# Kernel optimization log

Hardware: AMD Instinct MI355X
Metric: run time of the kernel (lower is better)

## Reference

```python
import jax, jax.numpy as jnp
import numpy as np

B, L, D, H, DK, DV = 2, 2048, 512, 8, 64, 64
EPS_LN = 1e-6


def setup_inputs() -> dict:
    key = jax.random.key(0)
    ks = jax.random.split(key, 14)
    ws = 0.02  # weight init scale
    inp = {}
    for i, n in enumerate(["q_r", "q_i", "k_r", "k_i", "v_r", "v_i"]):
        inp[n] = jax.random.normal(ks[i], (B, L, D), jnp.float32)
    for j, n in enumerate(["wq_r", "wq_i", "wk_r", "wk_i", "wv_r", "wv_i", "fc_r", "fc_i"]):
        inp[n] = jax.random.normal(ks[6 + j], (D, D), jnp.float32) * ws
    # complextorch CVLayerNorm affine: (2,2,D) weight, diag = 1/sqrt(2); complex bias = 0
    c = np.float32(1.0 / np.sqrt(2.0))
    ln_w = jnp.zeros((2, 2, D), jnp.float32).at[0, 0].set(c).at[1, 1].set(c)
    inp["ln_w"] = ln_w
    inp["ln_b_r"] = jnp.zeros((D,), jnp.float32)
    inp["ln_b_i"] = jnp.zeros((D,), jnp.float32)
    return inp


def _cv_layernorm(x, ln_w, ln_b_r, ln_b_i):
    # covariance-whitening complex LayerNorm over last dim (complextorch style)
    xr, xi = jnp.real(x), jnp.imag(x)
    xr = xr - jnp.mean(xr, axis=-1, keepdims=True)
    xi = xi - jnp.mean(xi, axis=-1, keepdims=True)
    vrr = jnp.mean(xr * xr, axis=-1, keepdims=True) + EPS_LN
    vii = jnp.mean(xi * xi, axis=-1, keepdims=True) + EPS_LN
    vri = jnp.mean(xr * xi, axis=-1, keepdims=True)
    s = jnp.sqrt(vrr * vii - vri * vri)
    t = jnp.sqrt(vrr + vii + 2.0 * s)
    inv = 1.0 / (s * t)
    rrr, rii, rri = (vii + s) * inv, (vrr + s) * inv, -vri * inv
    yr = rrr * xr + rri * xi
    yi = rri * xr + rii * xi
    out_r = ln_w[0, 0] * yr + ln_w[0, 1] * yi + ln_b_r
    out_i = ln_w[1, 0] * yr + ln_w[1, 1] * yi + ln_b_i
    return out_r, out_i


def _mha(q_r, q_i, k_r, k_i, v_r, v_i, wq_r, wq_i, wk_r, wk_i, wv_r, wv_i,
         fc_r, fc_i, ln_w, ln_b_r, ln_b_i):
    q = (q_r + 1j * q_i).astype(jnp.complex64)
    k = (k_r + 1j * k_i).astype(jnp.complex64)
    v = (v_r + 1j * v_i).astype(jnp.complex64)
    Wq = (wq_r + 1j * wq_i).astype(jnp.complex64)
    Wk = (wk_r + 1j * wk_i).astype(jnp.complex64)
    Wv = (wv_r + 1j * wv_i).astype(jnp.complex64)
    Wfc = (fc_r + 1j * fc_i).astype(jnp.complex64)
    b, lq = q.shape[0], q.shape[1]
    # complex linear projections (torch Linear: y = x @ W^T), split into heads
    qh = jnp.einsum('bld,ed->ble', q, Wq).reshape(b, lq, H, DK).transpose(0, 2, 1, 3)
    kh = jnp.einsum('bld,ed->ble', k, Wk).reshape(b, -1, H, DK).transpose(0, 2, 1, 3)
    vh = jnp.einsum('bld,ed->ble', v, Wv).reshape(b, -1, H, DV).transpose(0, 2, 1, 3)
    temp = jnp.float32(DK ** 0.5)
    attn = jnp.einsum('bhqd,bhkd->bhqk', qh / temp, kh)  # [B,H,Lq,Lk] complex
    # CVSoftMax: softmax over magnitude, phase preserved
    mag = jnp.abs(attn)
    w = jax.nn.softmax(mag, axis=-1)
    attn = (w * jnp.exp(1j * jnp.angle(attn))).astype(jnp.complex64)
    out = jnp.einsum('bhqk,bhkd->bhqd', attn, vh)
    out = out.transpose(0, 2, 1, 3).reshape(b, lq, H * DV)
    out = jnp.einsum('ble,de->bld', out, Wfc)
    x = out + q  # residual (dropout is identity at p=0 / eval)
    return _cv_layernorm(x, ln_w, ln_b_r, ln_b_i)


def reference(q_r, q_i, k_r, k_i, v_r, v_i, wq_r, wq_i, wk_r, wk_i, wv_r, wv_i,
              fc_r, fc_i, ln_w, ln_b_r, ln_b_i):
    out_r, out_i = _mha(q_r, q_i, k_r, k_i, v_r, v_i, wq_r, wq_i, wk_r, wk_i,
                        wv_r, wv_i, fc_r, fc_i, ln_w, ln_b_r, ln_b_i)
    # stack real/imag so output is a real float32 tensor [B, L, D, 2]
    return jnp.stack([out_r, out_i], axis=-1)
```

## Files before the change

### kernel.cpp

```cpp
#include <hip/hip_runtime.h>
#include <hip/hip_bf16.h>
#include <math.h>

#define NB 2
#define NL 2048
#define ND 512
#define NH 8
#define NDK 64
#define NROW (NB*NL)
#define HEADSZ (NB*NH*NL*NDK)
#define SEG_BIG ((size_t)NROW*ND)

typedef __attribute__((ext_vector_type(8))) short bf16x8;
typedef __attribute__((ext_vector_type(4))) float f32x4;

__device__ __align__(16) short g_bq_r[HEADSZ], g_bq_i[HEADSZ];
__device__ __align__(16) short g_bk_r[HEADSZ], g_bk_i[HEADSZ];
__device__ __align__(16) short g_bv_r[HEADSZ], g_bv_i[HEADSZ];
__device__ __align__(16) short g_bo_r[SEG_BIG], g_bo_i[SEG_BIG];
__device__ float g_x_r[SEG_BIG];
__device__ float g_x_i[SEG_BIG];
__device__ __align__(16) unsigned g_po[(size_t)2*16*NL*NDK];
__device__ float g_pw[(size_t)2*16*NL];

static __device__ __forceinline__ unsigned pack_bf2(float lo, float hi) {
    __hip_bfloat162 h = __float22bfloat162_rn(make_float2(lo, hi));
    unsigned u;
    __builtin_memcpy(&u, &h, 4);
    return u;
}
static __device__ __forceinline__ float bf_lo(unsigned u) {
    const unsigned v = u << 16;
    float f; __builtin_memcpy(&f, &v, 4);
    return f;
}
static __device__ __forceinline__ float bf_hi(unsigned u) {
    const unsigned v = u & 0xFFFF0000u;
    float f; __builtin_memcpy(&f, &v, 4);
    return f;
}
static __device__ __forceinline__ uint4 ld_cvt(const float* p) {
    const float4 a = *(const float4*)p;
    const float4 b = *(const float4*)(p + 4);
    uint4 o;
    o.x = pack_bf2(a.x, a.y); o.y = pack_bf2(a.z, a.w);
    o.z = pack_bf2(b.x, b.y); o.w = pack_bf2(b.z, b.w);
    return o;
}
static __device__ __forceinline__ bf16x8 negbf(bf16x8 v) {
    #pragma unroll
    for (int e = 0; e < 8; ++e) v[e] ^= (short)0x8000;
    return v;
}

struct GPtrs {
    const float* xr[3]; const float* xi[3];
    const float* wr[4]; const float* wi[4];
    const float* rr; const float* ri;
};

template<int MODE>
__global__ __launch_bounds__(256, 2)
void bgemm(GPtrs gp)
{
    __shared__ __align__(16) short sAr[64][64], sAi[64][64];
    __shared__ __align__(16) short sBr[64][64], sBi[64][64];

    const int bm = blockIdx.x, bn = blockIdx.y;
    const int which = (MODE == 0) ? blockIdx.z : 3;
    const int tx = threadIdx.x;
    const int wave = tx >> 6, lane = tx & 63;
    const int l15 = lane & 15, l4 = lane >> 4;

    const float* Xr = nullptr;
    const float* Xi = nullptr;
    if constexpr (MODE == 0) { Xr = gp.xr[which]; Xi = gp.xi[which]; }
    const float* Wr = gp.wr[which];
    const float* Wi = gp.wi[which];

    const int t0r = tx >> 3;
    const int t0g = tx & 7;

    f32x4 Cr[4] = {}, Ci[4] = {};

    for (int kk = 0; kk < ND; kk += 64) {
        uint4 va0, va1, va2, va3, vb0, vb1, vb2, vb3;
        {
            const size_t a0 = (size_t)(bm*64 + t0r)*ND + kk + t0g*8;
            const size_t a1 = a0 + (size_t)32*ND;
            if constexpr (MODE == 0) {
                va0 = ld_cvt(Xr + a0); va1 = ld_cvt(Xi + a0);
                va2 = ld_cvt(Xr + a1); va3 = ld_cvt(Xi + a1);
            } else {
                va0 = *(const uint4*)(g_bo_r + a0); va1 = *(const uint4*)(g_bo_i + a0);
                va2 = *(const uint4*)(g_bo_r + a1); va3 = *(const uint4*)(g_bo_i + a1);
            }
            const size_t b0 = (size_t)(bn*64 + t0r)*ND + kk + t0g*8;
            const size_t b1 = b0 + (size_t)32*ND;
            vb0 = ld_cvt(Wr + b0); vb1 = ld_cvt(Wi + b0);
            vb2 = ld_cvt(Wr + b1); vb3 = ld_cvt(Wi + b1);
        }
        __syncthreads();
        {
            const int g0 = (t0g ^ (t0r & 7)) << 3;
            const int g1 = (t0g ^ ((t0r + 32) & 7)) << 3;
            *(uint4*)&sAr[t0r][g0]    = va0;
            *(uint4*)&sAi[t0r][g0]    = va1;
            *(uint4*)&sAr[t0r+32][g1] = va2;
            *(uint4*)&sAi[t0r+32][g1] = va3;
            *(uint4*)&sBr[t0r][g0]    = vb0;
            *(uint4*)&sBi[t0r][g0]    = vb1;
            *(uint4*)&sBr[t0r+32][g1] = vb2;
            *(uint4*)&sBi[t0r+32][g1] = vb3;
        }
        __syncthreads();

        #pragma unroll
        for (int ks = 0; ks < 2; ++ks) {
            const int arow = 16*wave + l15;
            const int ag = ((ks*4 + l4) ^ (arow & 7)) << 3;
            const bf16x8 aAr = *(const bf16x8*)&sAr[arow][ag];
            const bf16x8 aAi = *(const bf16x8*)&sAi[arow][ag];
            const bf16x8 aAn = negbf(aAi);
            #pragma unroll
            for (int nt = 0; nt < 4; ++nt) {
                const int brow = nt*16 + l15;
                const int bg = ((ks*4 + l4) ^ (brow & 7)) << 3;
                const bf16x8 bBr = *(const bf16x8*)&sBr[brow][bg];
                const bf16x8 bBi = *(const bf16x8*)&sBi[brow][bg];
                Cr[nt] = __builtin_amdgcn_mfma_f32_16x16x32_bf16(aAr, bBr, Cr[nt], 0, 0, 0);
                Cr[nt] = __builtin_amdgcn_mfma_f32_16x16x32_bf16(aAn, bBi, Cr[nt], 0, 0, 0);
                Ci[nt] = __builtin_amdgcn_mfma_f32_16x16x32_bf16(aAr, bBi, Ci[nt], 0, 0, 0);
                Ci[nt] = __builtin_amdgcn_mfma_f32_16x16x32_bf16(aAi, bBr, Ci[nt], 0, 0, 0);
            }
        }
    }

    const int m0 = bm*64 + 16*wave + 4*l4;
    if constexpr (MODE == 0) {
        if (which == 2) {
            const int bb = m0 >> 11, ll = m0 & (NL-1);
            const int c = ll >> 5, lgrp = (ll >> 3) & 3, e = ll & 7;
            #pragma unroll
            for (int nt = 0; nt < 4; ++nt) {
                const int d = nt*16 + l15;
                const int r = d & 31, dpart = d >> 5;
                const int p = (4*dpart + lgrp) ^ (r & 7);
                const size_t off = (size_t)(bb*NH + bn)*(NL*NDK) + (size_t)c*2048 + (r*8 + p)*8 + e;
                *(uint2*)(g_bv_r + off) = make_uint2(pack_bf2(Cr[nt][0], Cr[nt][1]),
                                                     pack_bf2(Cr[nt][2], Cr[nt][3]));
                *(uint2*)(g_bv_i + off) = make_uint2(pack_bf2(Ci[nt][0], Ci[nt][1]),
                                                     pack_bf2(Ci[nt][2], Ci[nt][3]));
            }
        } else {
            const float s = (which == 0) ? 0.125f : 1.0f;
            short* Pr = (which == 0) ? g_bq_r : g_bk_r;
            short* Pi = (which == 0) ? g_bq_i : g_bk_i;
            #pragma unroll
            for (int r = 0; r < 4; ++r) {
                const int m = m0 + r;
                const int bb = m >> 11, ll = m & (NL-1);
                const size_t base = ((size_t)(bb*NH + bn)*NL + ll)*NDK;
                #pragma unroll
                for (int nt = 0; nt < 4; ++nt) {
                    int col = nt*16 + l15;
                    if (which == 1)
                        col = (col & 7) | ((((col >> 3) ^ (ll & 7))) << 3);
                    const unsigned pk = pack_bf2(Cr[nt][r]*s, Ci[nt][r]*s);
                    Pr[base + col] = (short)(pk & 0xFFFFu);
                    Pi[base + col] = (short)(pk >> 16);
                }
            }
        }
    } else {
        const float* Rr = gp.rr;
        const float* Ri = gp.ri;
        #pragma unroll
        for (int r = 0; r < 4; ++r) {
            const int m = m0 + r;
            const size_t base = (size_t)m*ND + bn*64;
            #pragma unroll
            for (int nt = 0; nt < 4; ++nt) {
                const size_t idx = base + nt*16 + l15;
                g_x_r[idx] = Cr[nt][r] + Rr[idx];
                g_x_i[idx] = Ci[nt][r] + Ri[idx];
            }
        }
    }
}

__global__ __launch_bounds__(256, 4)
void cattn()
{
    __shared__ __align__(16) short sKV[2][8192];
    __shared__ __align__(16) short sCr[64][32], sCi[64][32];

    const int nb = blockIdx.x;
    const int xcd = nb & 7, rest = nb >> 3;
    const int bh = xcd*2 + (rest >> 6);
    const int within = rest & 63;
    const int q0 = (within >> 1) * 64;
    const int half = within & 1;

    const int tx = threadIdx.x;
    const int wave = tx >> 6, lane = tx & 63;
    const int l15 = lane & 15, l4 = lane >> 4;

    const short* Kr = g_bk_r + (size_t)bh*NL*NDK;
    const short* Ki = g_bk_i + (size_t)bh*NL*NDK;
    const short* Vr = g_bv_r + (size_t)bh*NL*NDK;
    const short* Vi = g_bv_i + (size_t)bh*NL*NDK;

    bf16x8 aQr[2], aQi[2], aQn[2];
    {
        const size_t qb = ((size_t)bh*NL + q0 + 16*wave + l15)*NDK + 8*l4;
        aQr[0] = *(const bf16x8*)(g_bq_r + qb);
        aQr[1] = *(const bf16x8*)(g_bq_r + qb + 32);
        aQi[0] = *(const bf16x8*)(g_bq_i + qb);
        aQi[1] = *(const bf16x8*)(g_bq_i + qb + 32);
        aQn[0] = negbf(aQi[0]); aQn[1] = negbf(aQi[1]);
    }

    f32x4 Or[4] = {}, Oi[4] = {};
    float ws[4] = {0.f, 0.f, 0.f, 0.f};

    const short* kvplane = (wave == 0) ? Kr : (wave == 1) ? Ki : (wave == 2) ? Vr : Vi;
    const int pbase = wave * 2048;

    #define STAGE_KV(CHUNK, BUF) do {                                         \
        _Pragma("unroll")                                                     \
        for (int i_ = 0; i_ < 4; ++i_) {                                      \
            const int u_ = i_*64 + lane;                                      \
            __builtin_amdgcn_global_load_lds(                                 \
                (const __attribute__((address_space(1))) void*)               \
                    (kvplane + (size_t)(CHUNK)*2048 + (size_t)u_*8),          \
                (__attribute__((address_space(3))) void*)                     \
                    &sKV[BUF][pbase + u_*8], 16, 0, 0);                       \
        }                                                                     \
    } while (0)

    const int cbase = half * 32;
    STAGE_KV(cbase, 0);
    asm volatile("s_waitcnt vmcnt(0)" ::: "memory");
    __syncthreads();

    const float LOG2E = 1.44269504f;
    const float SHIFT = -4.0f*1.44269504f;

    for (int t = 0; t < 32; ++t) {
        const int cur = t & 1, nxt = cur ^ 1;
        if (t < 31) STAGE_KV(cbase + t + 1, nxt);

        #pragma unroll
        for (int tt = 0; tt < 2; ++tt) {
            const int row = tt*16 + l15;
            const int swb = row & 7;
            f32x4 Sr = {}, Si = {};
            __builtin_amdgcn_s_setprio(1);
            #pragma unroll
            for (int c = 0; c < 2; ++c) {
                const int off = (((c*4 + l4) ^ swb) << 3);
                const bf16x8 bKr = *(const bf16x8*)&sKV[cur][row*64 + off];
                const bf16x8 bKi = *(const bf16x8*)&sKV[cur][2048 + row*64 + off];
                Sr = __builtin_amdgcn_mfma_f32_16x16x32_bf16(aQr[c], bKr, Sr, 0, 0, 0);
                Sr = __builtin_amdgcn_mfma_f32_16x16x32_bf16(aQn[c], bKi, Sr, 0, 0, 0);
                Si = __builtin_amdgcn_mfma_f32_16x16x32_bf16(aQr[c], bKi, Si, 0, 0, 0);
                Si = __builtin_amdgcn_mfma_f32_16x16x32_bf16(aQi[c], bKr, Si, 0, 0, 0);
            }
            __builtin_amdgcn_s_setprio(0);
            const int kgrp = row >> 3;
            #pragma unroll
            for (int r = 0; r < 4; ++r) {
                const int qrow = 16*wave + 4*l4 + r;
                const float s2 = fmaxf(fmaf(Sr[r], Sr[r], Si[r]*Si[r]), 1e-30f);
                const float irs = __builtin_amdgcn_rsqf(s2);
                const float mag = s2 * irs;
                const float w = exp2f(fmaf(mag, LOG2E, SHIFT));
                const float sc = w * irs;
                ws[r] += w;
                const int col = (row & 7) | ((kgrp ^ ((qrow >> 2) & 3)) << 3);
                const unsigned pk = pack_bf2(Sr[r]*sc, Si[r]*sc);
                sCr[qrow][col] = (short)(pk & 0xFFFFu);
                sCi[qrow][col] = (short)(pk >> 16);
            }
        }

        asm volatile("s_waitcnt lgkmcnt(0)" ::: "memory");
        __builtin_amdgcn_sched_barrier(0);

        bf16x8 aCr, aCi, aCn;
        {
            const int qrow = 16*wave + l15;
            const int off = (l4 ^ ((qrow >> 2) & 3)) << 3;
            aCr = *(const bf16x8*)&sCr[qrow][off];
            aCi = *(const bf16x8*)&sCi[qrow][off];
            aCn = negbf(aCi);
        }
        __builtin_amdgcn_s_setprio(1);
        #pragma unroll
        for (int tt = 0; tt < 4; ++tt) {
            const int d = tt*16 + l15;
            const int r = d & 31, dpart = tt >> 1;
            const int p = (4*dpart + l4) ^ (r & 7);
            const int vb = r*64 + p*8;
            const bf16x8 bVr = *(const bf16x8*)&sKV[cur][4096 + vb];
            const bf16x8 bVi = *(const bf16x8*)&sKV[cur][6144 + vb];
            Or[tt] = __builtin_amdgcn_mfma_f32_16x16x32_bf16(aCr, bVr, Or[tt], 0, 0, 0);
            Or[tt] = __builtin_amdgcn_mfma_f32_16x16x32_bf16(aCn, bVi, Or[tt], 0, 0, 0);
            Oi[tt] = __builtin_amdgcn_mfma_f32_16x16x32_bf16(aCr, bVi, Oi[tt], 0, 0, 0);
            Oi[tt] = __builtin_amdgcn_mfma_f32_16x16x32_bf16(aCi, bVr, Oi[tt], 0, 0, 0);
        }
        __builtin_amdgcn_s_setprio(0);

        asm volatile("s_waitcnt vmcnt(0)" ::: "memory");
        __syncthreads();
    }

    #pragma unroll
    for (int r = 0; r < 4; ++r) {
        #pragma unroll
        for (int off = 8; off; off >>= 1) ws[r] += __shfl_xor(ws[r], off);
    }
    const size_t pb = (size_t)(half*16 + bh)*NL;
    if (l15 == 0) {
        #pragma unroll
        for (int r = 0; r < 4; ++r)
            g_pw[pb + q0 + 16*wave + 4*l4 + r] = ws[r];
    }
    #pragma unroll
    for (int tt = 0; tt < 4; ++tt) {
        const int d = tt*16 + l15;
        #pragma unroll
        for (int r = 0; r < 4; ++r) {
            const int q = q0 + 16*wave + 4*l4 + r;
            g_po[(pb + q)*NDK + d] = pack_bf2(Or[tt][r], Oi[tt][r]);
        }
    }
    #undef STAGE_KV
}

__global__ __launch_bounds__(256)
void comb()
{
    const size_t t4 = ((size_t)blockIdx.x*256 + threadIdx.x) * 4;
    const int d = (int)(t4 & 63);
    const int q = (int)((t4 >> 6) & (NL-1));
    const int bh = (int)(t4 >> 17);
    const size_t p = ((size_t)bh*NL + q)*NDK + d;
    const uint4 a = *(const uint4*)&g_po[p];
    const uint4 c = *(const uint4*)&g_po[(size_t)16*NL*NDK + p];
    const float w = g_pw[(size_t)bh*NL + q] + g_pw[(size_t)(16 + bh)*NL + q];
    const float inv = 1.0f / w;
    float fr[4], fi[4];
    fr[0] = (bf_lo(a.x) + bf_lo(c.x))*inv; fi[0] = (bf_hi(a.x) + bf_hi(c.x))*inv;
    fr[1] = (bf_lo(a.y) + bf_lo(c.y))*inv; fi[1] = (bf_hi(a.y) + bf_hi(c.y))*inv;
    fr[2] = (bf_lo(a.z) + bf_lo(c.z))*inv; fi[2] = (bf_hi(a.z) + bf_hi(c.z))*inv;
    fr[3] = (bf_lo(a.w) + bf_lo(c.w))*inv; fi[3] = (bf_hi(a.w) + bf_hi(c.w))*inv;
    const int b = bh >> 3, h = bh & 7;
    const size_t o = ((size_t)b*NL + q)*ND + h*NDK + d;
    *(uint2*)(g_bo_r + o) = make_uint2(pack_bf2(fr[0], fr[1]), pack_bf2(fr[2], fr[3]));
    *(uint2*)(g_bo_i + o) = make_uint2(pack_bf2(fi[0], fi[1]), pack_bf2(fi[2], fi[3]));
}

__global__ __launch_bounds__(256)
void cvln(const float* __restrict__ ln_w, const float* __restrict__ lnb_r,
          const float* __restrict__ lnb_i, float2* __restrict__ out)
{
    __shared__ float red[4][5];
    const int row = blockIdx.x, tx = threadIdx.x;
    const float* xr = g_x_r + (size_t)row*ND;
    const float* xi = g_x_i + (size_t)row*ND;
    const float a0 = xr[tx], a1 = xr[tx+256];
    const float b0 = xi[tx], b1 = xi[tx+256];
    float s_r = a0 + a1, s_i = b0 + b1;
    float srr = a0*a0 + a1*a1, sii = b0*b0 + b1*b1, sri = a0*b0 + a1*b1;
    #pragma unroll
    for (int off = 32; off; off >>= 1) {
        s_r += __shfl_xor(s_r, off);  s_i += __shfl_xor(s_i, off);
        srr += __shfl_xor(srr, off);  sii += __shfl_xor(sii, off);
        sri += __shfl_xor(sri, off);
    }
    const int wave = tx >> 6, lane = tx & 63;
    if (lane == 0) { red[wave][0]=s_r; red[wave][1]=s_i; red[wave][2]=srr; red[wave][3]=sii; red[wave][4]=sri; }
    __syncthreads();
    s_r = red[0][0]+red[1][0]+red[2][0]+red[3][0];
    s_i = red[0][1]+red[1][1]+red[2][1]+red[3][1];
    srr = red[0][2]+red[1][2]+red[2][2]+red[3][2];
    sii = red[0][3]+red[1][3]+red[2][3]+red[3][3];
    sri = red[0][4]+red[1][4]+red[2][4]+red[3][4];

    const float invD = 1.0f/ND;
    const float mr = s_r*invD, mi = s_i*invD;
    const float vrr = srr*invD - mr*mr + 1e-6f;
    const float vii = sii*invD - mi*mi + 1e-6f;
    const float vri = sri*invD - mr*mi;
    const float s  = sqrtf(vrr*vii - vri*vri);
    const float t  = sqrtf(vrr + vii + 2.0f*s);
    const float inv = 1.0f/(s*t);
    const float rrr = (vii + s)*inv, rii = (vrr + s)*inv, rri = -vri*inv;

    #pragma unroll
    for (int p = 0; p < 2; ++p) {
        const int d = tx + p*256;
        const float cxr = (p ? a1 : a0) - mr;
        const float cxi = (p ? b1 : b0) - mi;
        const float yr = rrr*cxr + rri*cxi;
        const float yi = rri*cxr + rii*cxi;
        const float w00 = ln_w[d], w01 = ln_w[512 + d];
        const float w10 = ln_w[1024 + d], w11 = ln_w[1536 + d];
        out[(size_t)row*ND + d] = make_float2(w00*yr + w01*yi + lnb_r[d],
                                              w10*yr + w11*yi + lnb_i[d]);
    }
}

extern "C" void kernel_launch(void* const* d_in, const int* in_sizes, int n_in,
                              void* d_out, int out_size, void* d_ws, size_t ws_size,
                              hipStream_t stream)
{
    (void)in_sizes; (void)n_in; (void)d_ws; (void)ws_size; (void)out_size;
    const float* ln_w = (const float*)d_in[14];
    const float* lnbr = (const float*)d_in[15];
    const float* lnbi = (const float*)d_in[16];

    GPtrs gp;
    gp.xr[0] = (const float*)d_in[0];  gp.xi[0] = (const float*)d_in[1];
    gp.xr[1] = (const float*)d_in[2];  gp.xi[1] = (const float*)d_in[3];
    gp.xr[2] = (const float*)d_in[4];  gp.xi[2] = (const float*)d_in[5];
    gp.wr[0] = (const float*)d_in[6];  gp.wi[0] = (const float*)d_in[7];
    gp.wr[1] = (const float*)d_in[8];  gp.wi[1] = (const float*)d_in[9];
    gp.wr[2] = (const float*)d_in[10]; gp.wi[2] = (const float*)d_in[11];
    gp.wr[3] = (const float*)d_in[12]; gp.wi[3] = (const float*)d_in[13];
    gp.rr = (const float*)d_in[0];     gp.ri = (const float*)d_in[1];

    bgemm<0><<<dim3(NROW/64, ND/64, 3), 256, 0, stream>>>(gp);
    cattn<<<1024, 256, 0, stream>>>();
    comb<<<2048, 256, 0, stream>>>();
    bgemm<1><<<dim3(NROW/64, ND/64), 256, 0, stream>>>(gp);
    cvln<<<NROW, 256, 0, stream>>>(ln_w, lnbr, lnbi, (float2*)d_out);
}
```

Measured before the change: 171.1 us.

## Enlarge complex GEMM M-tile to 128 rows with two MFMA row tiles per wave

The projection and output GEMMs now compute a 128x64 tile per block instead of 64x64. Each wave handles two 16-row A sub-tiles and reuses the B fragments it loads from shared memory across both. This cuts weight reloads from global memory and shared-memory B reads per MFMA, and halves the grid. The cost is more registers (accumulators doubled), more LDS, and fewer blocks (768 for the projection, 256 for the output GEMM), which may reduce occupancy and load balance.

```diff
diff --git a/kernel.cpp b/kernel.cpp
--- a/kernel.cpp
+++ b/kernel.cpp
@@ -63,8 +63,8 @@
 __global__ __launch_bounds__(256, 2)
 void bgemm(GPtrs gp)
 {
-    __shared__ __align__(16) short sAr[64][64], sAi[64][64];
-    __shared__ __align__(16) short sBr[64][64], sBi[64][64];
+    __shared__ __align__(16) short sAr[128][64], sAi[128][64];
+    __shared__ __align__(16) short sBr[64][64],  sBi[64][64];
 
     const int bm = blockIdx.x, bn = blockIdx.y;
     const int which = (MODE == 0) ? blockIdx.z : 3;
@@ -81,109 +81,123 @@
     const int t0r = tx >> 3;
     const int t0g = tx & 7;
 
-    f32x4 Cr[4] = {}, Ci[4] = {};
+    f32x4 Cr[2][4] = {}, Ci[2][4] = {};
 
     for (int kk = 0; kk < ND; kk += 64) {
-        uint4 va0, va1, va2, va3, vb0, vb1, vb2, vb3;
-        {
-            const size_t a0 = (size_t)(bm*64 + t0r)*ND + kk + t0g*8;
-            const size_t a1 = a0 + (size_t)32*ND;
+        uint4 va[8], vb[4];
+        #pragma unroll
+        for (int p = 0; p < 4; ++p) {
+            const size_t a = (size_t)(bm*128 + t0r + p*32)*ND + kk + t0g*8;
             if constexpr (MODE == 0) {
-                va0 = ld_cvt(Xr + a0); va1 = ld_cvt(Xi + a0);
-                va2 = ld_cvt(Xr + a1); va3 = ld_cvt(Xi + a1);
+                va[p]   = ld_cvt(Xr + a);
+                va[4+p] = ld_cvt(Xi + a);
             } else {
-                va0 = *(const uint4*)(g_bo_r + a0); va1 = *(const uint4*)(g_bo_i + a0);
-                va2 = *(const uint4*)(g_bo_r + a1); va3 = *(const uint4*)(g_bo_i + a1);
-            }
-            const size_t b0 = (size_t)(bn*64 + t0r)*ND + kk + t0g*8;
-            const size_t b1 = b0 + (size_t)32*ND;
-            vb0 = ld_cvt(Wr + b0); vb1 = ld_cvt(Wi + b0);
-            vb2 = ld_cvt(Wr + b1); vb3 = ld_cvt(Wi + b1);
+                va[p]   = *(const uint4*)(g_bo_r + a);
+                va[4+p] = *(const uint4*)(g_bo_i + a);
+            }
+        }
+        #pragma unroll
+        for (int p = 0; p < 2; ++p) {
+            const size_t bo = (size_t)(bn*64 + t0r + p*32)*ND + kk + t0g*8;
+            vb[p]   = ld_cvt(Wr + bo);
+            vb[2+p] = ld_cvt(Wi + bo);
         }
         __syncthreads();
-        {
-            const int g0 = (t0g ^ (t0r & 7)) << 3;
-            const int g1 = (t0g ^ ((t0r + 32) & 7)) << 3;
-            *(uint4*)&sAr[t0r][g0]    = va0;
-            *(uint4*)&sAi[t0r][g0]    = va1;
-            *(uint4*)&sAr[t0r+32][g1] = va2;
-            *(uint4*)&sAi[t0r+32][g1] = va3;
-            *(uint4*)&sBr[t0r][g0]    = vb0;
-            *(uint4*)&sBi[t0r][g0]    = vb1;
-            *(uint4*)&sBr[t0r+32][g1] = vb2;
-            *(uint4*)&sBi[t0r+32][g1] = vb3;
+        #pragma unroll
+        for (int p = 0; p < 4; ++p) {
+            const int row = t0r + p*32;
+            const int g = (t0g ^ (row & 7)) << 3;
+            *(uint4*)&sAr[row][g] = va[p];
+            *(uint4*)&sAi[row][g] = va[4+p];
+        }
+        #pragma unroll
+        for (int p = 0; p < 2; ++p) {
+            const int row = t0r + p*32;
+            const int g = (t0g ^ (row & 7)) << 3;
+            *(uint4*)&sBr[row][g] = vb[p];
+            *(uint4*)&sBi[row][g] = vb[2+p];
         }
         __syncthreads();
 
         #pragma unroll
         for (int ks = 0; ks < 2; ++ks) {
-            const int arow = 16*wave + l15;
-            const int ag = ((ks*4 + l4) ^ (arow & 7)) << 3;
-            const bf16x8 aAr = *(const bf16x8*)&sAr[arow][ag];
-            const bf16x8 aAi = *(const bf16x8*)&sAi[arow][ag];
-            const bf16x8 aAn = negbf(aAi);
+            bf16x8 bB_r[4], bB_i[4];
             #pragma unroll
             for (int nt = 0; nt < 4; ++nt) {
                 const int brow = nt*16 + l15;
                 const int bg = ((ks*4 + l4) ^ (brow & 7)) << 3;
-                const bf16x8 bBr = *(const bf16x8*)&sBr[brow][bg];
-                const bf16x8 bBi = *(const bf16x8*)&sBi[brow][bg];
-                Cr[nt] = __builtin_amdgcn_mfma_f32_16x16x32_bf16(aAr, bBr, Cr[nt], 0, 0, 0);
-                Cr[nt] = __builtin_amdgcn_mfma_f32_16x16x32_bf16(aAn, bBi, Cr[nt], 0, 0, 0);
-                Ci[nt] = __builtin_amdgcn_mfma_f32_16x16x32_bf16(aAr, bBi, Ci[nt], 0, 0, 0);
-                Ci[nt] = __builtin_amdgcn_mfma_f32_16x16x32_bf16(aAi, bBr, Ci[nt], 0, 0, 0);
-            }
-        }
-    }
-
-    const int m0 = bm*64 + 16*wave + 4*l4;
-    if constexpr (MODE == 0) {
-        if (which == 2) {
-            const int bb = m0 >> 11, ll = m0 & (NL-1);
-            const int c = ll >> 5, lgrp = (ll >> 3) & 3, e = ll & 7;
+                bB_r[nt] = *(const bf16x8*)&sBr[brow][bg];
+                bB_i[nt] = *(const bf16x8*)&sBi[brow][bg];
+            }
             #pragma unroll
-            for (int nt = 0; nt < 4; ++nt) {
-                const int d = nt*16 + l15;
-                const int r = d & 31, dpart = d >> 5;
-                const int p = (4*dpart + lgrp) ^ (r & 7);
-                const size_t off = (size_t)(bb*NH + bn)*(NL*NDK) + (size_t)c*2048 + (r*8 + p)*8 + e;
-                *(uint2*)(g_bv_r + off) = make_uint2(pack_bf2(Cr[nt][0], Cr[nt][1]),
-                                                     pack_bf2(Cr[nt][2], Cr[nt][3]));
-                *(uint2*)(g_bv_i + off) = make_uint2(pack_bf2(Ci[nt][0], Ci[nt][1]),
-                                                     pack_bf2(Ci[nt][2], Ci[nt][3]));
+            for (int mi = 0; mi < 2; ++mi) {
+                const int arow = 32*wave + 16*mi + l15;
+                const int ag = ((ks*4 + l4) ^ (arow & 7)) << 3;
+                const bf16x8 aAr = *(const bf16x8*)&sAr[arow][ag];
+                const bf16x8 aAi = *(const bf16x8*)&sAi[arow][ag];
+                const bf16x8 aAn = negbf(aAi);
+                #pragma unroll
+                for (int nt = 0; nt < 4; ++nt) {
+                    Cr[mi][nt] = __builtin_amdgcn_mfma_f32_16x16x32_bf16(aAr, bB_r[nt], Cr[mi][nt], 0, 0, 0);
+                    Cr[mi][nt] = __builtin_amdgcn_mfma_f32_16x16x32_bf16(aAn, bB_i[nt], Cr[mi][nt], 0, 0, 0);
+                    Ci[mi][nt] = __builtin_amdgcn_mfma_f32_16x16x32_bf16(aAr, bB_i[nt], Ci[mi][nt], 0, 0, 0);
+                    Ci[mi][nt] = __builtin_amdgcn_mfma_f32_16x16x32_bf16(aAi, bB_r[nt], Ci[mi][nt], 0, 0, 0);
+                }
+            }
+        }
+    }
+
+    #pragma unroll
+    for (int mi = 0; mi < 2; ++mi) {
+        const int m0 = bm*128 + 32*wave + 16*mi + 4*l4;
+        if constexpr (MODE == 0) {
+            if (which == 2) {
+                const int bb = m0 >> 11, ll = m0 & (NL-1);
+                const int c = ll >> 5, lgrp = (ll >> 3) & 3, e = ll & 7;
+                #pragma unroll
+                for (int nt = 0; nt < 4; ++nt) {
+                    const int d = nt*16 + l15;
+                    const int r = d & 31, dpart = d >> 5;
+                    const int p = (4*dpart + lgrp) ^ (r & 7);
+                    const size_t off = (size_t)(bb*NH + bn)*(NL*NDK) + (size_t)c*2048 + (r*8 + p)*8 + e;
+                    *(uint2*)(g_bv_r + off) = make_uint2(pack_bf2(Cr[mi][nt][0], Cr[mi][nt][1]),
+                                                         pack_bf2(Cr[mi][nt][2], Cr[mi][nt][3]));
+                    *(uint2*)(g_bv_i + off) = make_uint2(pack_bf2(Ci[mi][nt][0], Ci[mi][nt][1]),
+                                                         pack_bf2(Ci[mi][nt][2], Ci[mi][nt][3]));
+                }
+            } else {
+                const float s = (which == 0) ? 0.125f : 1.0f;
+                short* Pr = (which == 0) ? g_bq_r : g_bk_r;
+                short* Pi = (which == 0) ? g_bq_i : g_bk_i;
+                #pragma unroll
+                for (int r = 0; r < 4; ++r) {
+                    const int m = m0 + r;
+                    const int bb = m >> 11, ll = m & (NL-1);
+                    const size_t base = ((size_t)(bb*NH + bn)*NL + ll)*NDK;
+                    #pragma unroll
+                    for (int nt = 0; nt < 4; ++nt) {
+                        int col = nt*16 + l15;
+                        if (which == 1)
+                            col = (col & 7) | ((((col >> 3) ^ (ll & 7))) << 3);
+                        const unsigned pk = pack_bf2(Cr[mi][nt][r]*s, Ci[mi][nt][r]*s);
+                        Pr[base + col] = (short)(pk & 0xFFFFu);
+                        Pi[base + col] = (short)(pk >> 16);
+                    }
+                }
             }
         } else {
-            const float s = (which == 0) ? 0.125f : 1.0f;
-            short* Pr = (which == 0) ? g_bq_r : g_bk_r;
-            short* Pi = (which == 0) ? g_bq_i : g_bk_i;
+            const float* Rr = gp.rr;
+            const float* Ri = gp.ri;
             #pragma unroll
             for (int r = 0; r < 4; ++r) {
                 const int m = m0 + r;
-                const int bb = m >> 11, ll = m & (NL-1);
-                const size_t base = ((size_t)(bb*NH + bn)*NL + ll)*NDK;
+                const size_t base = (size_t)m*ND + bn*64;
                 #pragma unroll
                 for (int nt = 0; nt < 4; ++nt) {
-                    int col = nt*16 + l15;
-                    if (which == 1)
-                        col = (col & 7) | ((((col >> 3) ^ (ll & 7))) << 3);
-                    const unsigned pk = pack_bf2(Cr[nt][r]*s, Ci[nt][r]*s);
-                    Pr[base + col] = (short)(pk & 0xFFFFu);
-                    Pi[base + col] = (short)(pk >> 16);
+                    const size_t idx = base + nt*16 + l15;
+                    g_x_r[idx] = Cr[mi][nt][r] + Rr[idx];
+                    g_x_i[idx] = Ci[mi][nt][r] + Ri[idx];
                 }
-            }
-        }
-    } else {
-        const float* Rr = gp.rr;
-        const float* Ri = gp.ri;
-        #pragma unroll
-        for (int r = 0; r < 4; ++r) {
-            const int m = m0 + r;
-            const size_t base = (size_t)m*ND + bn*64;
-            #pragma unroll
-            for (int nt = 0; nt < 4; ++nt) {
-                const size_t idx = base + nt*16 + l15;
-                g_x_r[idx] = Cr[nt][r] + Rr[idx];
-                g_x_i[idx] = Ci[nt][r] + Ri[idx];
             }
         }
     }
@@ -432,9 +446,9 @@
     gp.wr[3] = (const float*)d_in[12]; gp.wi[3] = (const float*)d_in[13];
     gp.rr = (const float*)d_in[0];     gp.ri = (const float*)d_in[1];
 
-    bgemm<0><<<dim3(NROW/64, ND/64, 3), 256, 0, stream>>>(gp);
+    bgemm<0><<<dim3(NROW/128, ND/64, 3), 256, 0, stream>>>(gp);
     cattn<<<1024, 256, 0, stream>>>();
     comb<<<2048, 256, 0, stream>>>();
-    bgemm<1><<<dim3(NROW/64, ND/64), 256, 0, stream>>>(gp);
+    bgemm<1><<<dim3(NROW/128, ND/64), 256, 0, stream>>>(gp);
     cvln<<<NROW, 256, 0, stream>>>(ln_w, lnbr, lnbi, (float2*)d_out);
 }
```

New measurement: 212.5 us. 1.24x slower.

## Pre-convert inputs to pre-swizzled bf16 and stream GEMM tiles via global_load_lds

Applied to the files above, without the earlier changes.

Adds a conversion kernel that turns all fp32 activations and weights into bf16 once, storing them with the XOR swizzle already applied, and makes the combine kernel write its output in the same layout. The GEMM kernels then fill shared memory with direct global-to-LDS loads, one plane per wave, instead of per-thread fp32 loads, in-register conversion and LDS stores. This removes the repeated fp32 reads and conversions inside the projection GEMM. In exchange it adds an extra launch and a full read/write pass over the inputs, plus a trailing barrier per k-step.

```diff
diff --git a/kernel.cpp b/kernel.cpp
--- a/kernel.cpp
+++ b/kernel.cpp
@@ -10,10 +10,13 @@
 #define NROW (NB*NL)
 #define HEADSZ (NB*NH*NL*NDK)
 #define SEG_BIG ((size_t)NROW*ND)
+#define SEG_SMALL ((size_t)ND*ND)
+#define TOT_CVT (6*SEG_BIG + 8*SEG_SMALL)
 
 typedef __attribute__((ext_vector_type(8))) short bf16x8;
 typedef __attribute__((ext_vector_type(4))) float f32x4;
 
+__device__ __align__(16) short g_bf[TOT_CVT];
 __device__ __align__(16) short g_bq_r[HEADSZ], g_bq_i[HEADSZ];
 __device__ __align__(16) short g_bk_r[HEADSZ], g_bk_i[HEADSZ];
 __device__ __align__(16) short g_bv_r[HEADSZ], g_bv_i[HEADSZ];
@@ -53,18 +56,29 @@
     return v;
 }
 
-struct GPtrs {
-    const float* xr[3]; const float* xi[3];
-    const float* wr[4]; const float* wi[4];
-    const float* rr; const float* ri;
-};
+struct SrcPtrs { const float* p[14]; };
+
+__global__ __launch_bounds__(256)
+void tobf(SrcPtrs sp)
+{
+    const size_t i = ((size_t)blockIdx.x*256 + threadIdx.x) * 8;
+    if (i >= TOT_CVT) return;
+    int seg; size_t off, sbase;
+    if (i < 6*SEG_BIG) { seg = (int)(i / SEG_BIG); off = i % SEG_BIG; sbase = (size_t)seg*SEG_BIG; }
+    else { const size_t j = i - 6*SEG_BIG; seg = 6 + (int)(j / SEG_SMALL); off = j % SEG_SMALL;
+           sbase = 6*SEG_BIG + (size_t)(seg-6)*SEG_SMALL; }
+    const uint4 v = ld_cvt(sp.p[seg] + off);
+    const int r7 = (int)(off >> 9) & 7;
+    const int g  = (int)(off >> 3) & 7;
+    const size_t dst = (off & ~(size_t)0x38) | ((size_t)(g ^ r7) << 3);
+    *(uint4*)(g_bf + sbase + dst) = v;
+}
 
 template<int MODE>
 __global__ __launch_bounds__(256, 2)
-void bgemm(GPtrs gp)
-{
-    __shared__ __align__(16) short sAr[64][64], sAi[64][64];
-    __shared__ __align__(16) short sBr[64][64], sBi[64][64];
+void bgemm(const float* __restrict__ Rr, const float* __restrict__ Ri)
+{
+    __shared__ __align__(16) short sAB[16384];
 
     const int bm = blockIdx.x, bn = blockIdx.y;
     const int which = (MODE == 0) ? blockIdx.z : 3;
@@ -72,68 +86,50 @@
     const int wave = tx >> 6, lane = tx & 63;
     const int l15 = lane & 15, l4 = lane >> 4;
 
-    const float* Xr = nullptr;
-    const float* Xi = nullptr;
-    if constexpr (MODE == 0) { Xr = gp.xr[which]; Xi = gp.xi[which]; }
-    const float* Wr = gp.wr[which];
-    const float* Wi = gp.wi[which];
-
-    const int t0r = tx >> 3;
-    const int t0g = tx & 7;
+    const short* Xr = (MODE == 0) ? g_bf + (size_t)(2*which)*SEG_BIG   : g_bo_r;
+    const short* Xi = (MODE == 0) ? g_bf + (size_t)(2*which+1)*SEG_BIG : g_bo_i;
+    const short* Wr = g_bf + 6*SEG_BIG + (size_t)(2*which)*SEG_SMALL;
+    const short* Wi = g_bf + 6*SEG_BIG + (size_t)(2*which+1)*SEG_SMALL;
+
+    const short* plane = (wave == 0) ? Xr : (wave == 1) ? Xi : (wave == 2) ? Wr : Wi;
+    const int prow0 = ((wave < 2) ? bm : bn) * 64;
+    const int pbase = wave * 4096;
 
     f32x4 Cr[4] = {}, Ci[4] = {};
 
     for (int kk = 0; kk < ND; kk += 64) {
-        uint4 va0, va1, va2, va3, vb0, vb1, vb2, vb3;
-        {
-            const size_t a0 = (size_t)(bm*64 + t0r)*ND + kk + t0g*8;
-            const size_t a1 = a0 + (size_t)32*ND;
-            if constexpr (MODE == 0) {
-                va0 = ld_cvt(Xr + a0); va1 = ld_cvt(Xi + a0);
-                va2 = ld_cvt(Xr + a1); va3 = ld_cvt(Xi + a1);
-            } else {
-                va0 = *(const uint4*)(g_bo_r + a0); va1 = *(const uint4*)(g_bo_i + a0);
-                va2 = *(const uint4*)(g_bo_r + a1); va3 = *(const uint4*)(g_bo_i + a1);
-            }
-            const size_t b0 = (size_t)(bn*64 + t0r)*ND + kk + t0g*8;
-            const size_t b1 = b0 + (size_t)32*ND;
-            vb0 = ld_cvt(Wr + b0); vb1 = ld_cvt(Wi + b0);
-            vb2 = ld_cvt(Wr + b1); vb3 = ld_cvt(Wi + b1);
-        }
-        __syncthreads();
-        {
-            const int g0 = (t0g ^ (t0r & 7)) << 3;
-            const int g1 = (t0g ^ ((t0r + 32) & 7)) << 3;
-            *(uint4*)&sAr[t0r][g0]    = va0;
-            *(uint4*)&sAi[t0r][g0]    = va1;
-            *(uint4*)&sAr[t0r+32][g1] = va2;
-            *(uint4*)&sAi[t0r+32][g1] = va3;
-            *(uint4*)&sBr[t0r][g0]    = vb0;
-            *(uint4*)&sBi[t0r][g0]    = vb1;
-            *(uint4*)&sBr[t0r+32][g1] = vb2;
-            *(uint4*)&sBi[t0r+32][g1] = vb3;
-        }
+        #pragma unroll
+        for (int i_ = 0; i_ < 8; ++i_) {
+            const int u_ = i_*64 + lane;
+            __builtin_amdgcn_global_load_lds(
+                (const __attribute__((address_space(1))) void*)
+                    (plane + (size_t)(prow0 + (u_ >> 3))*ND + kk + (u_ & 7)*8),
+                (__attribute__((address_space(3))) void*)
+                    &sAB[pbase + u_*8], 16, 0, 0);
+        }
+        asm volatile("s_waitcnt vmcnt(0)" ::: "memory");
         __syncthreads();
 
         #pragma unroll
         for (int ks = 0; ks < 2; ++ks) {
             const int arow = 16*wave + l15;
             const int ag = ((ks*4 + l4) ^ (arow & 7)) << 3;
-            const bf16x8 aAr = *(const bf16x8*)&sAr[arow][ag];
-            const bf16x8 aAi = *(const bf16x8*)&sAi[arow][ag];
+            const bf16x8 aAr = *(const bf16x8*)&sAB[arow*64 + ag];
+            const bf16x8 aAi = *(const bf16x8*)&sAB[4096 + arow*64 + ag];
             const bf16x8 aAn = negbf(aAi);
             #pragma unroll
             for (int nt = 0; nt < 4; ++nt) {
                 const int brow = nt*16 + l15;
                 const int bg = ((ks*4 + l4) ^ (brow & 7)) << 3;
-                const bf16x8 bBr = *(const bf16x8*)&sBr[brow][bg];
-                const bf16x8 bBi = *(const bf16x8*)&sBi[brow][bg];
+                const bf16x8 bBr = *(const bf16x8*)&sAB[8192  + brow*64 + bg];
+                const bf16x8 bBi = *(const bf16x8*)&sAB[12288 + brow*64 + bg];
                 Cr[nt] = __builtin_amdgcn_mfma_f32_16x16x32_bf16(aAr, bBr, Cr[nt], 0, 0, 0);
                 Cr[nt] = __builtin_amdgcn_mfma_f32_16x16x32_bf16(aAn, bBi, Cr[nt], 0, 0, 0);
                 Ci[nt] = __builtin_amdgcn_mfma_f32_16x16x32_bf16(aAr, bBi, Ci[nt], 0, 0, 0);
                 Ci[nt] = __builtin_amdgcn_mfma_f32_16x16x32_bf16(aAi, bBr, Ci[nt], 0, 0, 0);
             }
         }
+        __syncthreads();
     }
 
     const int m0 = bm*64 + 16*wave + 4*l4;
@@ -173,8 +169,6 @@
             }
         }
     } else {
-        const float* Rr = gp.rr;
-        const float* Ri = gp.ri;
         #pragma unroll
         for (int r = 0; r < 4; ++r) {
             const int m = m0 + r;
@@ -357,7 +351,8 @@
     fr[2] = (bf_lo(a.z) + bf_lo(c.z))*inv; fi[2] = (bf_hi(a.z) + bf_hi(c.z))*inv;
     fr[3] = (bf_lo(a.w) + bf_lo(c.w))*inv; fi[3] = (bf_hi(a.w) + bf_hi(c.w))*inv;
     const int b = bh >> 3, h = bh & 7;
-    const size_t o = ((size_t)b*NL + q)*ND + h*NDK + d;
+    const int dsw = ((((d >> 3) ^ (q & 7))) << 3) | (d & 7);
+    const size_t o = ((size_t)b*NL + q)*ND + h*NDK + dsw;
     *(uint2*)(g_bo_r + o) = make_uint2(pack_bf2(fr[0], fr[1]), pack_bf2(fr[2], fr[3]));
     *(uint2*)(g_bo_i + o) = make_uint2(pack_bf2(fi[0], fi[1]), pack_bf2(fi[2], fi[3]));
 }
@@ -418,23 +413,20 @@
                               hipStream_t stream)
 {
     (void)in_sizes; (void)n_in; (void)d_ws; (void)ws_size; (void)out_size;
+    const float* q_r  = (const float*)d_in[0];
+    const float* q_i  = (const float*)d_in[1];
     const float* ln_w = (const float*)d_in[14];
     const float* lnbr = (const float*)d_in[15];
     const float* lnbi = (const float*)d_in[16];
 
-    GPtrs gp;
-    gp.xr[0] = (const float*)d_in[0];  gp.xi[0] = (const float*)d_in[1];
-    gp.xr[1] = (const float*)d_in[2];  gp.xi[1] = (const float*)d_in[3];
-    gp.xr[2] = (const float*)d_in[4];  gp.xi[2] = (const float*)d_in[5];
-    gp.wr[0] = (const float*)d_in[6];  gp.wi[0] = (const float*)d_in[7];
-    gp.wr[1] = (const float*)d_in[8];  gp.wi[1] = (const float*)d_in[9];
-    gp.wr[2] = (const float*)d_in[10]; gp.wi[2] = (const float*)d_in[11];
-    gp.wr[3] = (const float*)d_in[12]; gp.wi[3] = (const float*)d_in[13];
-    gp.rr = (const float*)d_in[0];     gp.ri = (const float*)d_in[1];
-
-    bgemm<0><<<dim3(NROW/64, ND/64, 3), 256, 0, stream>>>(gp);
+    SrcPtrs sp;
+    for (int j = 0; j < 14; ++j) sp.p[j] = (const float*)d_in[j];
+
+    const int cvt_blocks = (int)((TOT_CVT/8 + 255)/256);
+    tobf<<<cvt_blocks, 256, 0, stream>>>(sp);
+    bgemm<0><<<dim3(NROW/64, ND/64, 3), 256, 0, stream>>>(nullptr, nullptr);
     cattn<<<1024, 256, 0, stream>>>();
     comb<<<2048, 256, 0, stream>>>();
-    bgemm<1><<<dim3(NROW/64, ND/64), 256, 0, stream>>>(gp);
+    bgemm<1><<<dim3(NROW/64, ND/64), 256, 0, stream>>>(q_r, q_i);
     cvln<<<NROW, 256, 0, stream>>>(ln_w, lnbr, lnbi, (float2*)d_out);
 }
```

Result: no change. 168.3 us (-1.6%).

## Pre-swizzle weights to bf16 and load GEMM tiles via direct global-to-LDS

Applied to the files above, without the earlier changes.

A new kernel converts all eight weight matrices to bf16 once per call and stores them in the pre-swizzled LDS layout. The GEMMs then fetch those tiles straight into shared memory with global_load_lds instead of loading fp32, converting and storing through registers. The attention-combine kernel now writes its output pre-swizzled so the output projection can use the same direct path. The residual sum is stored as packed bf16 real/imag pairs instead of two fp32 arrays, which cuts traffic into the layer norm at some precision cost, and the extra launch plus added barriers add overhead.

```diff
diff --git a/kernel.cpp b/kernel.cpp
--- a/kernel.cpp
+++ b/kernel.cpp
@@ -10,16 +10,18 @@
 #define NROW (NB*NL)
 #define HEADSZ (NB*NH*NL*NDK)
 #define SEG_BIG ((size_t)NROW*ND)
+#define SEG_SMALL ((size_t)ND*ND)
+#define TOT_W (8*SEG_SMALL)
 
 typedef __attribute__((ext_vector_type(8))) short bf16x8;
 typedef __attribute__((ext_vector_type(4))) float f32x4;
 
+__device__ __align__(16) short g_bfw[TOT_W];
 __device__ __align__(16) short g_bq_r[HEADSZ], g_bq_i[HEADSZ];
 __device__ __align__(16) short g_bk_r[HEADSZ], g_bk_i[HEADSZ];
 __device__ __align__(16) short g_bv_r[HEADSZ], g_bv_i[HEADSZ];
 __device__ __align__(16) short g_bo_r[SEG_BIG], g_bo_i[SEG_BIG];
-__device__ float g_x_r[SEG_BIG];
-__device__ float g_x_i[SEG_BIG];
+__device__ __align__(16) unsigned g_x[SEG_BIG];
 __device__ __align__(16) unsigned g_po[(size_t)2*16*NL*NDK];
 __device__ float g_pw[(size_t)2*16*NL];
 
@@ -55,16 +57,29 @@
 
 struct GPtrs {
     const float* xr[3]; const float* xi[3];
-    const float* wr[4]; const float* wi[4];
     const float* rr; const float* ri;
 };
+struct WPtrs { const float* p[8]; };
+
+__global__ __launch_bounds__(256)
+void tobf(WPtrs wp)
+{
+    const size_t i = ((size_t)blockIdx.x*256 + threadIdx.x) * 8;
+    if (i >= TOT_W) return;
+    const int seg = (int)(i / SEG_SMALL);
+    const size_t off = i % SEG_SMALL;
+    const uint4 v = ld_cvt(wp.p[seg] + off);
+    const int r7 = (int)(off >> 9) & 7;
+    const int g  = (int)(off >> 3) & 7;
+    const size_t dst = (off & ~(size_t)0x38) | ((size_t)(g ^ r7) << 3);
+    *(uint4*)(g_bfw + (size_t)seg*SEG_SMALL + dst) = v;
+}
 
 template<int MODE>
 __global__ __launch_bounds__(256, 2)
 void bgemm(GPtrs gp)
 {
-    __shared__ __align__(16) short sAr[64][64], sAi[64][64];
-    __shared__ __align__(16) short sBr[64][64], sBi[64][64];
+    __shared__ __align__(16) short sAB[16384];
 
     const int bm = blockIdx.x, bn = blockIdx.y;
     const int which = (MODE == 0) ? blockIdx.z : 3;
@@ -75,8 +90,8 @@
     const float* Xr = nullptr;
     const float* Xi = nullptr;
     if constexpr (MODE == 0) { Xr = gp.xr[which]; Xi = gp.xi[which]; }
-    const float* Wr = gp.wr[which];
-    const float* Wi = gp.wi[which];
+    const short* Wr = g_bfw + (size_t)(2*which)*SEG_SMALL;
+    const short* Wi = g_bfw + (size_t)(2*which+1)*SEG_SMALL;
 
     const int t0r = tx >> 3;
     const int t0g = tx & 7;
@@ -84,56 +99,69 @@
     f32x4 Cr[4] = {}, Ci[4] = {};
 
     for (int kk = 0; kk < ND; kk += 64) {
-        uint4 va0, va1, va2, va3, vb0, vb1, vb2, vb3;
-        {
+        uint4 va0, va1, va2, va3;
+        if constexpr (MODE == 0) {
             const size_t a0 = (size_t)(bm*64 + t0r)*ND + kk + t0g*8;
             const size_t a1 = a0 + (size_t)32*ND;
-            if constexpr (MODE == 0) {
-                va0 = ld_cvt(Xr + a0); va1 = ld_cvt(Xi + a0);
-                va2 = ld_cvt(Xr + a1); va3 = ld_cvt(Xi + a1);
-            } else {
-                va0 = *(const uint4*)(g_bo_r + a0); va1 = *(const uint4*)(g_bo_i + a0);
-                va2 = *(const uint4*)(g_bo_r + a1); va3 = *(const uint4*)(g_bo_i + a1);
-            }
-            const size_t b0 = (size_t)(bn*64 + t0r)*ND + kk + t0g*8;
-            const size_t b1 = b0 + (size_t)32*ND;
-            vb0 = ld_cvt(Wr + b0); vb1 = ld_cvt(Wi + b0);
-            vb2 = ld_cvt(Wr + b1); vb3 = ld_cvt(Wi + b1);
-        }
-        __syncthreads();
-        {
+            va0 = ld_cvt(Xr + a0); va1 = ld_cvt(Xi + a0);
+            va2 = ld_cvt(Xr + a1); va3 = ld_cvt(Xi + a1);
+        }
+        if constexpr (MODE == 0) {
+            #pragma unroll
+            for (int i_ = 0; i_ < 4; ++i_) {
+                const int within = (i_ & 1)*256 + tx;
+                const short* plane = (i_ >> 1) ? Wi : Wr;
+                __builtin_amdgcn_global_load_lds(
+                    (const __attribute__((address_space(1))) void*)
+                        (plane + (size_t)(bn*64 + (within >> 3))*ND + kk + (within & 7)*8),
+                    (__attribute__((address_space(3))) void*)
+                        &sAB[8192 + (i_ >> 1)*4096 + within*8], 16, 0, 0);
+            }
+        } else {
+            #pragma unroll
+            for (int i_ = 0; i_ < 8; ++i_) {
+                const int within = (i_ & 1)*256 + tx;
+                const int pl = i_ >> 1;
+                const short* plane = (pl == 0) ? g_bo_r : (pl == 1) ? g_bo_i : (pl == 2) ? Wr : Wi;
+                const int row0 = (pl < 2) ? bm*64 : bn*64;
+                __builtin_amdgcn_global_load_lds(
+                    (const __attribute__((address_space(1))) void*)
+                        (plane + (size_t)(row0 + (within >> 3))*ND + kk + (within & 7)*8),
+                    (__attribute__((address_space(3))) void*)
+                        &sAB[pl*4096 + within*8], 16, 0, 0);
+            }
+        }
+        if constexpr (MODE == 0) {
             const int g0 = (t0g ^ (t0r & 7)) << 3;
             const int g1 = (t0g ^ ((t0r + 32) & 7)) << 3;
-            *(uint4*)&sAr[t0r][g0]    = va0;
-            *(uint4*)&sAi[t0r][g0]    = va1;
-            *(uint4*)&sAr[t0r+32][g1] = va2;
-            *(uint4*)&sAi[t0r+32][g1] = va3;
-            *(uint4*)&sBr[t0r][g0]    = vb0;
-            *(uint4*)&sBi[t0r][g0]    = vb1;
-            *(uint4*)&sBr[t0r+32][g1] = vb2;
-            *(uint4*)&sBi[t0r+32][g1] = vb3;
-        }
+            *(uint4*)&sAB[t0r*64 + g0]               = va0;
+            *(uint4*)&sAB[4096 + t0r*64 + g0]        = va1;
+            *(uint4*)&sAB[(t0r+32)*64 + g1]          = va2;
+            *(uint4*)&sAB[4096 + (t0r+32)*64 + g1]   = va3;
+        }
+        asm volatile("s_waitcnt vmcnt(0)" ::: "memory");
         __syncthreads();
 
         #pragma unroll
         for (int ks = 0; ks < 2; ++ks) {
             const int arow = 16*wave + l15;
             const int ag = ((ks*4 + l4) ^ (arow & 7)) << 3;
-            const bf16x8 aAr = *(const bf16x8*)&sAr[arow][ag];
-            const bf16x8 aAi = *(const bf16x8*)&sAi[arow][ag];
+            const bf16x8 aAr = *(const bf16x8*)&sAB[arow*64 + ag];
+            const bf16x8 aAi = *(const bf16x8*)&sAB[4096 + arow*64 + ag];
             const bf16x8 aAn = negbf(aAi);
             #pragma unroll
             for (int nt = 0; nt < 4; ++nt) {
                 const int brow = nt*16 + l15;
                 const int bg = ((ks*4 + l4) ^ (brow & 7)) << 3;
-                const bf16x8 bBr = *(const bf16x8*)&sBr[brow][bg];
-                const bf16x8 bBi = *(const bf16x8*)&sBi[brow][bg];
+                const bf16x8 bBr = *(const bf16x8*)&sAB[8192  + brow*64 + bg];
+                const bf16x8 bBi = *(const bf16x8*)&sAB[12288 + brow*64 + bg];
                 Cr[nt] = __builtin_amdgcn_mfma_f32_16x16x32_bf16(aAr, bBr, Cr[nt], 0, 0, 0);
                 Cr[nt] = __builtin_amdgcn_mfma_f32_16x16x32_bf16(aAn, bBi, Cr[nt], 0, 0, 0);
                 Ci[nt] = __builtin_amdgcn_mfma_f32_16x16x32_bf16(aAr, bBi, Ci[nt], 0, 0, 0);
                 Ci[nt] = __builtin_amdgcn_mfma_f32_16x16x32_bf16(aAi, bBr, Ci[nt], 0, 0, 0);
             }
         }
+        __syncthreads();
     }
 
     const int m0 = bm*64 + 16*wave + 4*l4;
@@ -182,8 +210,7 @@
             #pragma unroll
             for (int nt = 0; nt < 4; ++nt) {
                 const size_t idx = base + nt*16 + l15;
-                g_x_r[idx] = Cr[nt][r] + Rr[idx];
-                g_x_i[idx] = Ci[nt][r] + Ri[idx];
+                g_x[idx] = pack_bf2(Cr[nt][r] + Rr[idx], Ci[nt][r] + Ri[idx]);
             }
         }
     }
@@ -357,7 +384,8 @@
     fr[2] = (bf_lo(a.z) + bf_lo(c.z))*inv; fi[2] = (bf_hi(a.z) + bf_hi(c.z))*inv;
     fr[3] = (bf_lo(a.w) + bf_lo(c.w))*inv; fi[3] = (bf_hi(a.w) + bf_hi(c.w))*inv;
     const int b = bh >> 3, h = bh & 7;
-    const size_t o = ((size_t)b*NL + q)*ND + h*NDK + d;
+    const int dsw = ((((d >> 3) ^ (q & 7))) << 3) | (d & 7);
+    const size_t o = ((size_t)b*NL + q)*ND + h*NDK + dsw;
     *(uint2*)(g_bo_r + o) = make_uint2(pack_bf2(fr[0], fr[1]), pack_bf2(fr[2], fr[3]));
     *(uint2*)(g_bo_i + o) = make_uint2(pack_bf2(fi[0], fi[1]), pack_bf2(fi[2], fi[3]));
 }
@@ -368,10 +396,10 @@
 {
     __shared__ float red[4][5];
     const int row = blockIdx.x, tx = threadIdx.x;
-    const float* xr = g_x_r + (size_t)row*ND;
-    const float* xi = g_x_i + (size_t)row*ND;
-    const float a0 = xr[tx], a1 = xr[tx+256];
-    const float b0 = xi[tx], b1 = xi[tx+256];
+    const unsigned* xp = g_x + (size_t)row*ND;
+    const unsigned u0 = xp[tx], u1 = xp[tx + 256];
+    const float a0 = bf_lo(u0), a1 = bf_lo(u1);
+    const float b0 = bf_hi(u0), b1 = bf_hi(u1);
     float s_r = a0 + a1, s_i = b0 + b1;
     float srr = a0*a0 + a1*a1, sii = b0*b0 + b1*b1, sri = a0*b0 + a1*b1;
     #pragma unroll
@@ -426,12 +454,13 @@
     gp.xr[0] = (const float*)d_in[0];  gp.xi[0] = (const float*)d_in[1];
     gp.xr[1] = (const float*)d_in[2];  gp.xi[1] = (const float*)d_in[3];
     gp.xr[2] = (const float*)d_in[4];  gp.xi[2] = (const float*)d_in[5];
-    gp.wr[0] = (const float*)d_in[6];  gp.wi[0] = (const float*)d_in[7];
-    gp.wr[1] = (const float*)d_in[8];  gp.wi[1] = (const float*)d_in[9];
-    gp.wr[2] = (const float*)d_in[10]; gp.wi[2] = (const float*)d_in[11];
-    gp.wr[3] = (const float*)d_in[12]; gp.wi[3] = (const float*)d_in[13];
     gp.rr = (const float*)d_in[0];     gp.ri = (const float*)d_in[1];
 
+    WPtrs wp;
+    for (int j = 0; j < 8; ++j) wp.p[j] = (const float*)d_in[6 + j];
+
+    const int wcvt_blocks = (int)((TOT_W/8 + 255)/256);
+    tobf<<<wcvt_blocks, 256, 0, stream>>>(wp);
     bgemm<0><<<dim3(NROW/64, ND/64, 3), 256, 0, stream>>>(gp);
     cattn<<<1024, 256, 0, stream>>>();
     comb<<<2048, 256, 0, stream>>>();
```

After: 162.4 us. 1.05x faster.
